# Optimization experiments

Hardware: AMD Instinct MI355X
Metric: run time of the kernel (lower is better)

The kernel has to match this reference:

```python
import jax, jax.numpy as jnp
import numpy as np

N_NODES = 50000
N_EDGES = 800000


def gcn_conv(x, edge_index, W, b):
    """PyG GCNConv: add self-loops, symmetric deg^{-1/2} normalization,
    dense transform, scatter-add aggregation."""
    n = x.shape[0]
    src, dst = edge_index[0], edge_index[1]
    # add self-loops
    loop = jnp.arange(n, dtype=src.dtype)
    src = jnp.concatenate([src, loop])
    dst = jnp.concatenate([dst, loop])
    # degree on destination nodes (includes self-loops -> deg >= 1)
    deg = jax.ops.segment_sum(jnp.ones_like(dst, dtype=x.dtype), dst, num_segments=n)
    dinv = jax.lax.rsqrt(deg)
    norm = dinv[src] * dinv[dst]  # [E+N]
    h = x @ W                     # [N, F_out] dense GEMM
    msg = h[src] * norm[:, None]  # gather + scale, [E+N, F_out]
    out = jax.ops.segment_sum(msg, dst, num_segments=n)  # scatter-add
    return out + b


def setup_inputs() -> dict:
    key = jax.random.key(0)
    ks = jax.random.split(key, 8)
    x = jax.random.normal(ks[0], (N_NODES, 100), dtype=jnp.float32)
    edge_index = jax.random.randint(ks[1], (2, N_EDGES), 0, N_NODES, dtype=jnp.int64)
    W1 = jax.random.normal(ks[2], (100, 256), dtype=jnp.float32) * 0.1
    b1 = jnp.zeros((256,), dtype=jnp.float32)
    W2 = jax.random.normal(ks[3], (256, 128), dtype=jnp.float32) * 0.06
    b2 = jnp.zeros((128,), dtype=jnp.float32)
    Wfc = jax.random.normal(ks[4], (128, 1), dtype=jnp.float32) * 0.09
    bfc = jnp.zeros((1,), dtype=jnp.float32)
    return {"x": x, "edge_index": edge_index, "W1": W1, "b1": b1,
            "W2": W2, "b2": b2, "Wfc": Wfc, "bfc": bfc}


def reference(x, edge_index, W1, b1, W2, b2, Wfc, bfc):
    # eval mode: F.dropout with training=False is identity
    h = jax.nn.relu(gcn_conv(x, edge_index, W1, b1))
    h = jax.nn.relu(gcn_conv(h, edge_index, W2, b2))
    return h @ Wfc + bfc  # [N, 1]
```

## Files before the change

### kernel.cpp

```cpp
#include <hip/hip_runtime.h>
#include <hip/hip_bf16.h>


#define F0 100
#define F1 256
#define F2 128
#define CAP 2048

typedef _Float16 f16x4 __attribute__((ext_vector_type(4)));
typedef _Float16 f16x8 __attribute__((ext_vector_type(8)));
typedef float f32x4 __attribute__((ext_vector_type(4)));


__global__ void zero_i32(int* p, int n) {
    int i = blockIdx.x * blockDim.x + threadIdx.x;
    if (i < n) p[i] = 0;
}

__global__ void fill_f32(float* out, const float* __restrict__ bfc, int n) {
    int i = blockIdx.x * blockDim.x + threadIdx.x;
    if (i < n) out[i] = bfc[0];
}

__global__ void deg_count_i(const int* __restrict__ dst, int* deg, int e) {
    int i = blockIdx.x * blockDim.x + threadIdx.x;
    if (i < e) atomicAdd(deg + dst[i], 1);
}

__global__ __launch_bounds__(256) void scan1(const int* __restrict__ deg,
                                             int* __restrict__ excl,
                                             int* __restrict__ bsum,
                                             float* __restrict__ dinv, int n) {
    __shared__ int wsum[4];
    int i = blockIdx.x * 256 + threadIdx.x;
    int lane = threadIdx.x & 63, wid = threadIdx.x >> 6;
    int v = (i < n) ? deg[i] : 0;
    if (i < n) dinv[i] = rsqrtf((float)(v + 1));
    int s = v;
#pragma unroll
    for (int off = 1; off < 64; off <<= 1) {
        int t = __shfl_up(s, off, 64);
        if (lane >= off) s += t;
    }
    if (lane == 63) wsum[wid] = s;
    __syncthreads();
    int add = 0;
    for (int w = 0; w < wid; w++) add += wsum[w];
    if (i < n) excl[i] = add + s - v;
    if (threadIdx.x == 255) bsum[blockIdx.x] = add + s;
}

__global__ __launch_bounds__(256) void scan2(int* __restrict__ bsum, int nb,
                                             int* __restrict__ rowptr, int n) {
    __shared__ int wsum[4];
    int lane = threadIdx.x & 63, wid = threadIdx.x >> 6;
    int v = (threadIdx.x < nb) ? bsum[threadIdx.x] : 0;
    int s = v;
#pragma unroll
    for (int off = 1; off < 64; off <<= 1) {
        int t = __shfl_up(s, off, 64);
        if (lane >= off) s += t;
    }
    if (lane == 63) wsum[wid] = s;
    __syncthreads();
    int add = 0;
    for (int w = 0; w < wid; w++) add += wsum[w];
    if (threadIdx.x < nb) bsum[threadIdx.x] = add + s - v;
    if (threadIdx.x == 255) rowptr[n] = add + s;
}

__global__ void scan3(const int* __restrict__ excl, const int* __restrict__ bsum,
                      int* __restrict__ rowptr, int* __restrict__ cursor, int n) {
    int i = blockIdx.x * 256 + threadIdx.x;
    if (i < n) {
        int r = excl[i] + bsum[blockIdx.x];
        rowptr[i] = r;
        cursor[i] = r;
    }
}

__global__ void csr_fill(const int* __restrict__ src, const int* __restrict__ dst,
                         int* cursor, int* __restrict__ csr, int e) {
    int i = blockIdx.x * blockDim.x + threadIdx.x;
    if (i < e) {
        int pos = atomicAdd(cursor + dst[i], 1);
        csr[pos] = src[i];
    }
}

__global__ void scale_x(const float4* __restrict__ x4,
                        const float* __restrict__ dinv,
                        float4* __restrict__ xs4, int n25) {
    int i = blockIdx.x * blockDim.x + threadIdx.x;
    if (i < n25) {
        float d = dinv[i / 25];
        float4 v = x4[i];
        v.x *= d; v.y *= d; v.z *= d; v.w *= d;
        xs4[i] = v;
    }
}

__global__ void wprep(const float* __restrict__ W1, const float* __restrict__ W2,
                      _Float16* __restrict__ W1h, _Float16* __restrict__ W1l,
                      _Float16* __restrict__ W2h, _Float16* __restrict__ W2l) {
    int i = blockIdx.x * 256 + threadIdx.x;
    if (i < 256 * 128) {
        int c = i >> 7, k = i & 127;
        float v = (k < F0) ? W1[(size_t)k * F1 + c] : 0.f;
        _Float16 h = (_Float16)v;
        W1h[i] = h;
        W1l[i] = (_Float16)(v - (float)h);
    } else if (i < 256 * 128 + 128 * 256) {
        int j = i - 256 * 128;
        int c = j >> 8, k = j & 255;
        float v = W2[(size_t)k * F2 + c];
        _Float16 h = (_Float16)v;
        W2h[j] = h;
        W2l[j] = (_Float16)(v - (float)h);
    }
}


__global__ __launch_bounds__(256) void pull_f100(
        const float* __restrict__ xs, const int* __restrict__ rowptr,
        const int* __restrict__ csr, const float* __restrict__ dinv,
        _Float16* __restrict__ aggh, _Float16* __restrict__ aggl, int n) {
    int wave = threadIdx.x >> 6, lane = threadIdx.x & 63;
    int v = blockIdx.x * 4 + wave;
    if (v >= n) return;
    int beg = rowptr[v], end = rowptr[v + 1];
    float dv = dinv[v];
    int half = lane >> 5, q = lane & 31;
    bool act = q < 25;
    float4 acc = {0.f, 0.f, 0.f, 0.f};
    if (half == 0 && act) acc = ((const float4*)(xs + (size_t)v * F0))[q];

    for (int base = beg; base < end; base += 64) {
        int cnt = min(64, end - base);
        int sidx = (lane < cnt) ? csr[base + lane] : 0;
        int npf = cnt >> 1;
        int p = 0;
        for (; p + 4 <= npf; p += 4) {
            int s0 = __shfl(sidx, 2 * p + half, 64);
            int s1 = __shfl(sidx, 2 * p + 2 + half, 64);
            int s2 = __shfl(sidx, 2 * p + 4 + half, 64);
            int s3 = __shfl(sidx, 2 * p + 6 + half, 64);
            if (act) {
                float4 r0 = ((const float4*)(xs + (size_t)s0 * F0))[q];
                float4 r1 = ((const float4*)(xs + (size_t)s1 * F0))[q];
                float4 r2 = ((const float4*)(xs + (size_t)s2 * F0))[q];
                float4 r3 = ((const float4*)(xs + (size_t)s3 * F0))[q];
                acc.x += (r0.x + r1.x) + (r2.x + r3.x);
                acc.y += (r0.y + r1.y) + (r2.y + r3.y);
                acc.z += (r0.z + r1.z) + (r2.z + r3.z);
                acc.w += (r0.w + r1.w) + (r2.w + r3.w);
            }
        }
        for (; p < npf; p++) {
            int s0 = __shfl(sidx, 2 * p + half, 64);
            if (act) {
                float4 r0 = ((const float4*)(xs + (size_t)s0 * F0))[q];
                acc.x += r0.x; acc.y += r0.y; acc.z += r0.z; acc.w += r0.w;
            }
        }
        if (cnt & 1) {
            int sl = __shfl(sidx, cnt - 1, 64);
            if (half == 0 && act) {
                float4 r = ((const float4*)(xs + (size_t)sl * F0))[q];
                acc.x += r.x; acc.y += r.y; acc.z += r.z; acc.w += r.w;
            }
        }
    }
    float ox = __shfl_down(acc.x, 32, 64);
    float oy = __shfl_down(acc.y, 32, 64);
    float oz = __shfl_down(acc.z, 32, 64);
    float ow = __shfl_down(acc.w, 32, 64);
    if (half == 0) {
        float4 r = {0.f, 0.f, 0.f, 0.f};
        if (act) {
            r.x = dv * (acc.x + ox);
            r.y = dv * (acc.y + oy);
            r.z = dv * (acc.z + oz);
            r.w = dv * (acc.w + ow);
        }
        f16x4 hh, ll;
        hh[0] = (_Float16)r.x; ll[0] = (_Float16)(r.x - (float)hh[0]);
        hh[1] = (_Float16)r.y; ll[1] = (_Float16)(r.y - (float)hh[1]);
        hh[2] = (_Float16)r.z; ll[2] = (_Float16)(r.z - (float)hh[2]);
        hh[3] = (_Float16)r.w; ll[3] = (_Float16)(r.w - (float)hh[3]);
        *(f16x4*)(aggh + (size_t)v * 128 + 4 * q) = hh;
        *(f16x4*)(aggl + (size_t)v * 128 + 4 * q) = ll;
    }
}

__global__ __launch_bounds__(512) void gemm12_fused(
        const _Float16* __restrict__ Ah, const _Float16* __restrict__ Al,
        const _Float16* __restrict__ W1h, const _Float16* __restrict__ W1l,
        const _Float16* __restrict__ W2h, const _Float16* __restrict__ W2l,
        const float* __restrict__ b1, const float* __restrict__ dinv,
        float* __restrict__ C, int n) {
    __shared__ _Float16 sAh[128][136], sAl[128][136];
    int tid = threadIdx.x, lane = tid & 63, wave = tid >> 6;
    int wm = wave >> 2, wn = wave & 3;
    int r0 = blockIdx.x * 128;
    int lr = lane & 15, kg = lane >> 4, ks8 = kg * 8;

    f32x4 acc1[4][4] = {};
    int arow[4];
#pragma unroll
    for (int i = 0; i < 4; ++i) arow[i] = min(r0 + wm * 64 + i * 16 + lr, n - 1);

#pragma unroll
    for (int k0 = 0; k0 < 128; k0 += 32) {
        f16x8 a_h[4], a_l[4], b_h[4], b_l[4];
#pragma unroll
        for (int i = 0; i < 4; ++i) {
            a_h[i] = *(const f16x8*)(Ah + (size_t)arow[i] * 128 + k0 + ks8);
            a_l[i] = *(const f16x8*)(Al + (size_t)arow[i] * 128 + k0 + ks8);
        }
#pragma unroll
        for (int j = 0; j < 4; ++j) {
            int col = wn * 64 + j * 16 + lr;
            b_h[j] = *(const f16x8*)(W1h + (size_t)col * 128 + k0 + ks8);
            b_l[j] = *(const f16x8*)(W1l + (size_t)col * 128 + k0 + ks8);
        }
#pragma unroll
        for (int i = 0; i < 4; ++i)
#pragma unroll
            for (int j = 0; j < 4; ++j) {
                acc1[i][j] = __builtin_amdgcn_mfma_f32_16x16x32_f16(a_l[i], b_h[j], acc1[i][j], 0, 0, 0);
                acc1[i][j] = __builtin_amdgcn_mfma_f32_16x16x32_f16(a_h[i], b_l[j], acc1[i][j], 0, 0, 0);
                acc1[i][j] = __builtin_amdgcn_mfma_f32_16x16x32_f16(a_h[i], b_h[j], acc1[i][j], 0, 0, 0);
            }
    }
#pragma unroll
    for (int j = 0; j < 4; ++j) {
        float bv = b1[wn * 64 + j * 16 + lr];
#pragma unroll
        for (int i = 0; i < 4; ++i)
#pragma unroll
            for (int r = 0; r < 4; ++r)
                acc1[i][j][r] = fmaxf(acc1[i][j][r] + bv, 0.f);
    }

    f32x4 acc2[4][2] = {};
#pragma unroll
    for (int half = 0; half < 2; ++half) {
        if (half) __syncthreads();
        if ((wn >> 1) == half) {
            int cb = (wn & 1) * 64;
#pragma unroll
            for (int i = 0; i < 4; ++i)
#pragma unroll
                for (int j = 0; j < 4; ++j)
#pragma unroll
                    for (int r = 0; r < 4; ++r) {
                        int row = wm * 64 + i * 16 + kg * 4 + r;
                        int col = cb + j * 16 + lr;
                        float v = acc1[i][j][r];
                        _Float16 h = (_Float16)v;
                        sAh[row][col] = h;
                        sAl[row][col] = (_Float16)(v - (float)h);
                    }
        }
        __syncthreads();
#pragma unroll
        for (int k0 = 0; k0 < 128; k0 += 32) {
            f16x8 a_h[4], a_l[4], b_h[2], b_l[2];
#pragma unroll
            for (int i = 0; i < 4; ++i) {
                a_h[i] = *(const f16x8*)&sAh[wm * 64 + i * 16 + lr][k0 + ks8];
                a_l[i] = *(const f16x8*)&sAl[wm * 64 + i * 16 + lr][k0 + ks8];
            }
#pragma unroll
            for (int j = 0; j < 2; ++j) {
                int col = wn * 32 + j * 16 + lr;
                int kk = half * 128 + k0 + ks8;
                b_h[j] = *(const f16x8*)(W2h + (size_t)col * 256 + kk);
                b_l[j] = *(const f16x8*)(W2l + (size_t)col * 256 + kk);
            }
#pragma unroll
            for (int i = 0; i < 4; ++i)
#pragma unroll
                for (int j = 0; j < 2; ++j) {
                    acc2[i][j] = __builtin_amdgcn_mfma_f32_16x16x32_f16(a_l[i], b_h[j], acc2[i][j], 0, 0, 0);
                    acc2[i][j] = __builtin_amdgcn_mfma_f32_16x16x32_f16(a_h[i], b_l[j], acc2[i][j], 0, 0, 0);
                    acc2[i][j] = __builtin_amdgcn_mfma_f32_16x16x32_f16(a_h[i], b_h[j], acc2[i][j], 0, 0, 0);
                }
        }
    }

#pragma unroll
    for (int i = 0; i < 4; ++i)
#pragma unroll
        for (int r = 0; r < 4; ++r) {
            int gr = r0 + wm * 64 + i * 16 + kg * 4 + r;
            if (gr < n) {
                float d = dinv[gr];
#pragma unroll
                for (int j = 0; j < 2; ++j) {
                    int chunk = wn * 2 + j;
                    C[((size_t)chunk * n + gr) * 16 + lr] = acc2[i][j][r] * d;
                }
            }
        }
}


__global__ __launch_bounds__(256) void pull_c16_fused(
        const float* __restrict__ h2c, const int* __restrict__ rowptr,
        const int* __restrict__ csr, const float* __restrict__ dinv,
        const float* __restrict__ b2, const float* __restrict__ Wfc,
        float* __restrict__ out, int n) {
    __shared__ int s_row[65];
    __shared__ float s_dinv[64];
    __shared__ int s_csr[CAP];
    int chunk = blockIdx.x & 7;
    int nb = blockIdx.x >> 3;
    int v0 = nb * 64;
    int tid = threadIdx.x;
    int lane = tid & 63, wv = tid >> 6;
    int q = lane & 3;
    int g2 = (lane >> 2) & 3;
    int grp = lane >> 4;
    const float* __restrict__ tab = h2c + (size_t)chunk * n * 16;

    if (tid <= 64) s_row[tid] = rowptr[min(v0 + tid, n)];
    if (tid < 64) s_dinv[tid] = (v0 + tid < n) ? dinv[v0 + tid] : 0.f;
    __syncthreads();
    int ebeg = s_row[0], eend = s_row[64];

    int base_local = wv * 16 + grp * 4;

    float4 acc[4];
#pragma unroll
    for (int nn = 0; nn < 4; ++nn) acc[nn] = (float4){0.f, 0.f, 0.f, 0.f};

#pragma unroll
    for (int nn = 0; nn < 4; ++nn) {
        int node = v0 + base_local + nn;
        if (node < n && g2 == 0)
            acc[nn] = ((const float4*)(tab + (size_t)node * 16))[q];
    }

    for (int w0 = ebeg; w0 < eend; w0 += CAP) {
        int wcnt = min(CAP, eend - w0);
        if (w0 != ebeg) __syncthreads();
        for (int i = tid; i < wcnt; i += 256)
            s_csr[i] = __builtin_nontemporal_load(csr + w0 + i);
        __syncthreads();
#pragma unroll
        for (int nn = 0; nn < 4; ++nn) {
            int local = base_local + nn;
            int nbg = max(s_row[local], w0) - w0;
            int nen = min(s_row[local + 1], w0 + wcnt) - w0;
            for (int t = nbg + 4 * g2; t < nen; t += 16) {
                int i1 = min(t + 1, nen - 1);
                int i2 = min(t + 2, nen - 1);
                int i3 = min(t + 3, nen - 1);
                int s0 = s_csr[t];
                int s1 = s_csr[i1];
                int s2 = s_csr[i2];
                int s3 = s_csr[i3];
                float4 r0 = ((const float4*)(tab + (size_t)s0 * 16))[q];
                float4 r1 = ((const float4*)(tab + (size_t)s1 * 16))[q];
                float4 r2 = ((const float4*)(tab + (size_t)s2 * 16))[q];
                float4 r3 = ((const float4*)(tab + (size_t)s3 * 16))[q];
                bool m1 = (t + 1 < nen), m2 = (t + 2 < nen), m3 = (t + 3 < nen);
                acc[nn].x += r0.x + (m1 ? r1.x : 0.f);
                acc[nn].y += r0.y + (m1 ? r1.y : 0.f);
                acc[nn].z += r0.z + (m1 ? r1.z : 0.f);
                acc[nn].w += r0.w + (m1 ? r1.w : 0.f);
                acc[nn].x += (m2 ? r2.x : 0.f) + (m3 ? r3.x : 0.f);
                acc[nn].y += (m2 ? r2.y : 0.f) + (m3 ? r3.y : 0.f);
                acc[nn].z += (m2 ? r2.z : 0.f) + (m3 ? r3.z : 0.f);
                acc[nn].w += (m2 ? r2.w : 0.f) + (m3 ? r3.w : 0.f);
            }
        }
    }

    int c0 = chunk * 16 + 4 * q;
    float4 bb = *(const float4*)(b2 + c0);
    float4 ww = *(const float4*)(Wfc + c0);
#pragma unroll
    for (int nn = 0; nn < 4; ++nn) {
        int local = base_local + nn;
        int node = v0 + local;
        float dv = s_dinv[local];
        float4 a = acc[nn];
        a.x += __shfl_xor(a.x, 4, 64);
        a.y += __shfl_xor(a.y, 4, 64);
        a.z += __shfl_xor(a.z, 4, 64);
        a.w += __shfl_xor(a.w, 4, 64);
        a.x += __shfl_xor(a.x, 8, 64);
        a.y += __shfl_xor(a.y, 8, 64);
        a.z += __shfl_xor(a.z, 8, 64);
        a.w += __shfl_xor(a.w, 8, 64);
        float part = fmaxf(fmaf(dv, a.x, bb.x), 0.f) * ww.x
                   + fmaxf(fmaf(dv, a.y, bb.y), 0.f) * ww.y
                   + fmaxf(fmaf(dv, a.z, bb.z), 0.f) * ww.z
                   + fmaxf(fmaf(dv, a.w, bb.w), 0.f) * ww.w;
        part += __shfl_xor(part, 1, 64);
        part += __shfl_xor(part, 2, 64);
        if (node < n && (lane & 15) == 0) atomicAdd(out + node, part);
    }
}


extern "C" void kernel_launch(void* const* d_in, const int* in_sizes, int n_in,
                              void* d_out, int out_size, void* d_ws, size_t ws_size,
                              hipStream_t stream) {
    const float* x   = (const float*)d_in[0];
    const int*   ei  = (const int*)d_in[1];
    const float* W1  = (const float*)d_in[2];
    const float* b1  = (const float*)d_in[3];
    const float* W2  = (const float*)d_in[4];
    const float* b2  = (const float*)d_in[5];
    const float* Wfc = (const float*)d_in[6];
    const float* bfc = (const float*)d_in[7];
    float* out = (float*)d_out;

    const int n = in_sizes[0] / F0;
    const int e = in_sizes[1] / 2;
    const int* src = ei;
    const int* dst = ei + e;

    char* wsb = (char*)d_ws;
    size_t off = 0;
    auto alloc = [&](size_t bytes) -> void* {
        off = (off + 255) & ~(size_t)255;
        void* r = wsb + off;
        off += bytes;
        return r;
    };
    int* deg    = (int*)alloc((size_t)n * 4);
    int* excl   = (int*)alloc((size_t)n * 4);
    int* bsum   = (int*)alloc(1024);
    int* rowptr = (int*)alloc((size_t)(n + 1) * 4);
    int* cursor = (int*)alloc((size_t)n * 4);
    int* csr    = (int*)alloc((size_t)e * 4);
    float* dinv = (float*)alloc((size_t)n * 4);
    _Float16* W1h = (_Float16*)alloc(256 * 128 * 2);
    _Float16* W1l = (_Float16*)alloc(256 * 128 * 2);
    _Float16* W2h = (_Float16*)alloc(128 * 256 * 2);
    _Float16* W2l = (_Float16*)alloc(128 * 256 * 2);
    char* bufA = (char*)alloc((size_t)n * 128 * 4);
    float* xs  = (float*)bufA;
    float* h2c = (float*)bufA;
    _Float16* aggh = (_Float16*)alloc((size_t)n * 128 * 2);
    _Float16* aggl = (_Float16*)alloc((size_t)n * 128 * 2);

    const int B = 256;
    const int nb = (n + B - 1) / B;
    const int rblocks = (n + 127) / 128;

    zero_i32<<<nb, B, 0, stream>>>(deg, n);
    fill_f32<<<nb, B, 0, stream>>>(out, bfc, n);
    deg_count_i<<<(e + B - 1) / B, B, 0, stream>>>(dst, deg, e);
    scan1<<<nb, B, 0, stream>>>(deg, excl, bsum, dinv, n);
    scale_x<<<((n * 25) + B - 1) / B, B, 0, stream>>>(
        (const float4*)x, dinv, (float4*)xs, n * 25);
    wprep<<<256, 256, 0, stream>>>(W1, W2, W1h, W1l, W2h, W2l);
    scan2<<<1, B, 0, stream>>>(bsum, nb, rowptr, n);
    scan3<<<nb, B, 0, stream>>>(excl, bsum, rowptr, cursor, n);
    csr_fill<<<(e + B - 1) / B, B, 0, stream>>>(src, dst, cursor, csr, e);

    pull_f100<<<(n + 3) / 4, 256, 0, stream>>>(xs, rowptr, csr, dinv, aggh, aggl, n);
    gemm12_fused<<<rblocks, 512, 0, stream>>>(aggh, aggl, W1h, W1l, W2h, W2l,
                                              b1, dinv, h2c, n);
    pull_c16_fused<<<8 * ((n + 63) / 64), 256, 0, stream>>>(
        h2c, rowptr, csr, dinv, b2, Wfc, out, n);
}
```

Measured before the change: 343.5 us.

## Use row-major h2 with wave-per-node pull and shrink GEMM2 LDS staging

The second aggregation now reads a row-major [N,128] h2 table, with one wave per node and half-waves gathering alternate neighbours as float4 rows. This replaces the 8-chunk column-split layout, the shared-memory CSR staging and the atomic accumulation into out. The final bias is written directly, which removes the fill kernel and the atomics. The fused GEMM stages the layer-1 activations in four 64-column passes, halving the LDS footprint to raise occupancy, at the cost of extra barriers.

```diff
diff --git a/kernel.cpp b/kernel.cpp
--- a/kernel.cpp
+++ b/kernel.cpp
@@ -5,7 +5,6 @@
 #define F0 100
 #define F1 256
 #define F2 128
-#define CAP 2048
 
 typedef _Float16 f16x4 __attribute__((ext_vector_type(4)));
 typedef _Float16 f16x8 __attribute__((ext_vector_type(8)));
@@ -15,11 +14,6 @@
 __global__ void zero_i32(int* p, int n) {
     int i = blockIdx.x * blockDim.x + threadIdx.x;
     if (i < n) p[i] = 0;
-}
-
-__global__ void fill_f32(float* out, const float* __restrict__ bfc, int n) {
-    int i = blockIdx.x * blockDim.x + threadIdx.x;
-    if (i < n) out[i] = bfc[0];
 }
 
 __global__ void deg_count_i(const int* __restrict__ dst, int* deg, int e) {
@@ -199,7 +193,7 @@
         const _Float16* __restrict__ W2h, const _Float16* __restrict__ W2l,
         const float* __restrict__ b1, const float* __restrict__ dinv,
         float* __restrict__ C, int n) {
-    __shared__ _Float16 sAh[128][136], sAl[128][136];
+    __shared__ _Float16 sAh[128][72], sAl[128][72];
     int tid = threadIdx.x, lane = tid & 63, wave = tid >> 6;
     int wm = wave >> 2, wn = wave & 3;
     int r0 = blockIdx.x * 128;
@@ -245,10 +239,9 @@
 
     f32x4 acc2[4][2] = {};
 #pragma unroll
-    for (int half = 0; half < 2; ++half) {
-        if (half) __syncthreads();
-        if ((wn >> 1) == half) {
-            int cb = (wn & 1) * 64;
+    for (int pass = 0; pass < 4; ++pass) {
+        if (pass) __syncthreads();
+        if (wn == pass) {
 #pragma unroll
             for (int i = 0; i < 4; ++i)
 #pragma unroll
@@ -256,7 +249,7 @@
 #pragma unroll
                     for (int r = 0; r < 4; ++r) {
                         int row = wm * 64 + i * 16 + kg * 4 + r;
-                        int col = cb + j * 16 + lr;
+                        int col = j * 16 + lr;
                         float v = acc1[i][j][r];
                         _Float16 h = (_Float16)v;
                         sAh[row][col] = h;
@@ -265,7 +258,7 @@
         }
         __syncthreads();
 #pragma unroll
-        for (int k0 = 0; k0 < 128; k0 += 32) {
+        for (int k0 = 0; k0 < 64; k0 += 32) {
             f16x8 a_h[4], a_l[4], b_h[2], b_l[2];
 #pragma unroll
             for (int i = 0; i < 4; ++i) {
@@ -275,7 +268,7 @@
 #pragma unroll
             for (int j = 0; j < 2; ++j) {
                 int col = wn * 32 + j * 16 + lr;
-                int kk = half * 128 + k0 + ks8;
+                int kk = pass * 64 + k0 + ks8;
                 b_h[j] = *(const f16x8*)(W2h + (size_t)col * 256 + kk);
                 b_l[j] = *(const f16x8*)(W2l + (size_t)col * 256 + kk);
             }
@@ -299,110 +292,78 @@
                 float d = dinv[gr];
 #pragma unroll
                 for (int j = 0; j < 2; ++j) {
-                    int chunk = wn * 2 + j;
-                    C[((size_t)chunk * n + gr) * 16 + lr] = acc2[i][j][r] * d;
+                    int col = (wn * 2 + j) * 16 + lr;
+                    C[(size_t)gr * F2 + col] = acc2[i][j][r] * d;
                 }
             }
         }
 }
 
-
-__global__ __launch_bounds__(256) void pull_c16_fused(
-        const float* __restrict__ h2c, const int* __restrict__ rowptr,
+__global__ __launch_bounds__(256) void pull_f128_fused(
+        const float* __restrict__ h2s, const int* __restrict__ rowptr,
         const int* __restrict__ csr, const float* __restrict__ dinv,
         const float* __restrict__ b2, const float* __restrict__ Wfc,
-        float* __restrict__ out, int n) {
-    __shared__ int s_row[65];
-    __shared__ float s_dinv[64];
-    __shared__ int s_csr[CAP];
-    int chunk = blockIdx.x & 7;
-    int nb = blockIdx.x >> 3;
-    int v0 = nb * 64;
-    int tid = threadIdx.x;
-    int lane = tid & 63, wv = tid >> 6;
-    int q = lane & 3;
-    int g2 = (lane >> 2) & 3;
-    int grp = lane >> 4;
-    const float* __restrict__ tab = h2c + (size_t)chunk * n * 16;
-
-    if (tid <= 64) s_row[tid] = rowptr[min(v0 + tid, n)];
-    if (tid < 64) s_dinv[tid] = (v0 + tid < n) ? dinv[v0 + tid] : 0.f;
-    __syncthreads();
-    int ebeg = s_row[0], eend = s_row[64];
-
-    int base_local = wv * 16 + grp * 4;
-
-    float4 acc[4];
-#pragma unroll
-    for (int nn = 0; nn < 4; ++nn) acc[nn] = (float4){0.f, 0.f, 0.f, 0.f};
-
-#pragma unroll
-    for (int nn = 0; nn < 4; ++nn) {
-        int node = v0 + base_local + nn;
-        if (node < n && g2 == 0)
-            acc[nn] = ((const float4*)(tab + (size_t)node * 16))[q];
-    }
-
-    for (int w0 = ebeg; w0 < eend; w0 += CAP) {
-        int wcnt = min(CAP, eend - w0);
-        if (w0 != ebeg) __syncthreads();
-        for (int i = tid; i < wcnt; i += 256)
-            s_csr[i] = __builtin_nontemporal_load(csr + w0 + i);
-        __syncthreads();
-#pragma unroll
-        for (int nn = 0; nn < 4; ++nn) {
-            int local = base_local + nn;
-            int nbg = max(s_row[local], w0) - w0;
-            int nen = min(s_row[local + 1], w0 + wcnt) - w0;
-            for (int t = nbg + 4 * g2; t < nen; t += 16) {
-                int i1 = min(t + 1, nen - 1);
-                int i2 = min(t + 2, nen - 1);
-                int i3 = min(t + 3, nen - 1);
-                int s0 = s_csr[t];
-                int s1 = s_csr[i1];
-                int s2 = s_csr[i2];
-                int s3 = s_csr[i3];
-                float4 r0 = ((const float4*)(tab + (size_t)s0 * 16))[q];
-                float4 r1 = ((const float4*)(tab + (size_t)s1 * 16))[q];
-                float4 r2 = ((const float4*)(tab + (size_t)s2 * 16))[q];
-                float4 r3 = ((const float4*)(tab + (size_t)s3 * 16))[q];
-                bool m1 = (t + 1 < nen), m2 = (t + 2 < nen), m3 = (t + 3 < nen);
-                acc[nn].x += r0.x + (m1 ? r1.x : 0.f);
-                acc[nn].y += r0.y + (m1 ? r1.y : 0.f);
-                acc[nn].z += r0.z + (m1 ? r1.z : 0.f);
-                acc[nn].w += r0.w + (m1 ? r1.w : 0.f);
-                acc[nn].x += (m2 ? r2.x : 0.f) + (m3 ? r3.x : 0.f);
-                acc[nn].y += (m2 ? r2.y : 0.f) + (m3 ? r3.y : 0.f);
-                acc[nn].z += (m2 ? r2.z : 0.f) + (m3 ? r3.z : 0.f);
-                acc[nn].w += (m2 ? r2.w : 0.f) + (m3 ? r3.w : 0.f);
-            }
-        }
-    }
-
-    int c0 = chunk * 16 + 4 * q;
-    float4 bb = *(const float4*)(b2 + c0);
-    float4 ww = *(const float4*)(Wfc + c0);
-#pragma unroll
-    for (int nn = 0; nn < 4; ++nn) {
-        int local = base_local + nn;
-        int node = v0 + local;
-        float dv = s_dinv[local];
-        float4 a = acc[nn];
-        a.x += __shfl_xor(a.x, 4, 64);
-        a.y += __shfl_xor(a.y, 4, 64);
-        a.z += __shfl_xor(a.z, 4, 64);
-        a.w += __shfl_xor(a.w, 4, 64);
-        a.x += __shfl_xor(a.x, 8, 64);
-        a.y += __shfl_xor(a.y, 8, 64);
-        a.z += __shfl_xor(a.z, 8, 64);
-        a.w += __shfl_xor(a.w, 8, 64);
-        float part = fmaxf(fmaf(dv, a.x, bb.x), 0.f) * ww.x
-                   + fmaxf(fmaf(dv, a.y, bb.y), 0.f) * ww.y
-                   + fmaxf(fmaf(dv, a.z, bb.z), 0.f) * ww.z
-                   + fmaxf(fmaf(dv, a.w, bb.w), 0.f) * ww.w;
-        part += __shfl_xor(part, 1, 64);
-        part += __shfl_xor(part, 2, 64);
-        if (node < n && (lane & 15) == 0) atomicAdd(out + node, part);
+        const float* __restrict__ bfc, float* __restrict__ out, int n) {
+    int wave = threadIdx.x >> 6, lane = threadIdx.x & 63;
+    int v = blockIdx.x * 4 + wave;
+    if (v >= n) return;
+    int beg = rowptr[v], end = rowptr[v + 1];
+    float dv = dinv[v];
+    int half = lane >> 5, q = lane & 31;
+    float4 acc = {0.f, 0.f, 0.f, 0.f};
+    if (half == 0) acc = ((const float4*)(h2s + (size_t)v * F2))[q];
+
+    for (int base = beg; base < end; base += 64) {
+        int cnt = min(64, end - base);
+        int sidx = (lane < cnt) ? csr[base + lane] : 0;
+        int npf = cnt >> 1;
+        int p = 0;
+        for (; p + 4 <= npf; p += 4) {
+            int s0 = __shfl(sidx, 2 * p + half, 64);
+            int s1 = __shfl(sidx, 2 * p + 2 + half, 64);
+            int s2 = __shfl(sidx, 2 * p + 4 + half, 64);
+            int s3 = __shfl(sidx, 2 * p + 6 + half, 64);
+            float4 r0 = ((const float4*)(h2s + (size_t)s0 * F2))[q];
+            float4 r1 = ((const float4*)(h2s + (size_t)s1 * F2))[q];
+            float4 r2 = ((const float4*)(h2s + (size_t)s2 * F2))[q];
+            float4 r3 = ((const float4*)(h2s + (size_t)s3 * F2))[q];
+            acc.x += (r0.x + r1.x) + (r2.x + r3.x);
+            acc.y += (r0.y + r1.y) + (r2.y + r3.y);
+            acc.z += (r0.z + r1.z) + (r2.z + r3.z);
+            acc.w += (r0.w + r1.w) + (r2.w + r3.w);
+        }
+        for (; p < npf; p++) {
+            int s0 = __shfl(sidx, 2 * p + half, 64);
+            float4 r0 = ((const float4*)(h2s + (size_t)s0 * F2))[q];
+            acc.x += r0.x; acc.y += r0.y; acc.z += r0.z; acc.w += r0.w;
+        }
+        if (cnt & 1) {
+            int sl = __shfl(sidx, cnt - 1, 64);
+            if (half == 0) {
+                float4 r = ((const float4*)(h2s + (size_t)sl * F2))[q];
+                acc.x += r.x; acc.y += r.y; acc.z += r.z; acc.w += r.w;
+            }
+        }
+    }
+    float ox = __shfl_down(acc.x, 32, 64);
+    float oy = __shfl_down(acc.y, 32, 64);
+    float oz = __shfl_down(acc.z, 32, 64);
+    float ow = __shfl_down(acc.w, 32, 64);
+    if (half == 0) {
+        float4 b2v = ((const float4*)b2)[q];
+        float4 wv = ((const float4*)Wfc)[q];
+        float t0 = dv * (acc.x + ox);
+        float t1 = dv * (acc.y + oy);
+        float t2 = dv * (acc.z + oz);
+        float t3 = dv * (acc.w + ow);
+        float part = fmaxf(t0 + b2v.x, 0.f) * wv.x + fmaxf(t1 + b2v.y, 0.f) * wv.y +
+                     fmaxf(t2 + b2v.z, 0.f) * wv.z + fmaxf(t3 + b2v.w, 0.f) * wv.w;
+        part += __shfl_down(part, 16, 64);
+        part += __shfl_down(part, 8, 64);
+        part += __shfl_down(part, 4, 64);
+        part += __shfl_down(part, 2, 64);
+        part += __shfl_down(part, 1, 64);
+        if (lane == 0) out[v] = part + bfc[0];
     }
 }
 
@@ -445,17 +406,15 @@
     _Float16* W2h = (_Float16*)alloc(128 * 256 * 2);
     _Float16* W2l = (_Float16*)alloc(128 * 256 * 2);
     char* bufA = (char*)alloc((size_t)n * 128 * 4);
-    float* xs  = (float*)bufA;
-    float* h2c = (float*)bufA;
+    float* xs = (float*)bufA;
+    float* h2 = (float*)bufA;
     _Float16* aggh = (_Float16*)alloc((size_t)n * 128 * 2);
     _Float16* aggl = (_Float16*)alloc((size_t)n * 128 * 2);
 
     const int B = 256;
     const int nb = (n + B - 1) / B;
-    const int rblocks = (n + 127) / 128;
 
     zero_i32<<<nb, B, 0, stream>>>(deg, n);
-    fill_f32<<<nb, B, 0, stream>>>(out, bfc, n);
     deg_count_i<<<(e + B - 1) / B, B, 0, stream>>>(dst, deg, e);
     scan1<<<nb, B, 0, stream>>>(deg, excl, bsum, dinv, n);
     scale_x<<<((n * 25) + B - 1) / B, B, 0, stream>>>(
@@ -466,8 +425,8 @@
     csr_fill<<<(e + B - 1) / B, B, 0, stream>>>(src, dst, cursor, csr, e);
 
     pull_f100<<<(n + 3) / 4, 256, 0, stream>>>(xs, rowptr, csr, dinv, aggh, aggl, n);
-    gemm12_fused<<<rblocks, 512, 0, stream>>>(aggh, aggl, W1h, W1l, W2h, W2l,
-                                              b1, dinv, h2c, n);
-    pull_c16_fused<<<8 * ((n + 63) / 64), 256, 0, stream>>>(
-        h2c, rowptr, csr, dinv, b2, Wfc, out, n);
-}
+    gemm12_fused<<<(n + 127) / 128, 512, 0, stream>>>(aggh, aggl, W1h, W1l,
+                                                      W2h, W2l, b1, dinv, h2, n);
+    pull_f128_fused<<<(n + 3) / 4, 256, 0, stream>>>(h2, rowptr, csr, dinv,
+                                                     b2, Wfc, bfc, out, n);
+}
```

New measurement: 339.3 us. Within noise of the previous version (-1.2%).
